# Performance work log

Hardware: AMD Instinct MI355X
Metric: run time of the kernel (lower is better)

The kernel has to match this reference:

```python
import jax, jax.numpy as jnp
import numpy as np

C_IN, C_OUT = 128, 128
B, H, W = 16, 192, 192


def _conv(x, w, pad):
    # x: NCHW, w: OIHW, pad: ((ph,ph),(pw,pw))
    return jax.lax.conv_general_dilated(
        x, w, window_strides=(1, 1), padding=pad,
        dimension_numbers=('NCHW', 'OIHW', 'NCHW'))


def _diag_masks(dtype=jnp.float32):
    eye = jnp.eye(3, dtype=dtype)            # mask_19: mask[c, c] = 1
    anti = eye[::-1, :]                      # mask_37: mask[2-c, c] = 1
    return eye[None, None], anti[None, None] # broadcast to (O,I,3,3)


def setup_inputs() -> dict:
    key = jax.random.key(0)
    ks = jax.random.split(key, 6)
    return {
        'x': jax.random.normal(ks[0], (B, C_IN, H, W), dtype=jnp.float32),
        'w_square': jax.random.normal(ks[1], (C_OUT, C_IN, 3, 3), dtype=jnp.float32) * 0.05,
        'w_ver': jax.random.normal(ks[2], (C_OUT, C_IN, 3, 1), dtype=jnp.float32) * 0.05,
        'w_hor': jax.random.normal(ks[3], (C_OUT, C_IN, 1, 3), dtype=jnp.float32) * 0.05,
        'w_diag19': jax.random.normal(ks[4], (C_OUT, C_IN, 3, 3), dtype=jnp.float32) * 0.05,
        'w_diag37': jax.random.normal(ks[5], (C_OUT, C_IN, 3, 3), dtype=jnp.float32) * 0.05,
    }


def reference(x, w_square, w_ver, w_hor, w_diag19, w_diag37):
    m19, m37 = _diag_masks(x.dtype)
    out = _conv(x, w_square, ((1, 1), (1, 1)))
    out = out + _conv(x, w_ver, ((1, 1), (0, 0)))
    out = out + _conv(x, w_hor, ((0, 0), (1, 1)))
    out = out + _conv(x, w_diag19 * m19, ((1, 1), (1, 1)))
    out = out + _conv(x, w_diag37 * m37, ((1, 1), (1, 1)))
    return out
```

## Files before the change

kernel.cpp:

```cpp
#include <hip/hip_runtime.h>

#define HH 192
#define WW 192
#define HWPIX (HH * WW)
#define PLANE 5184
#define CHUNKB 20736

typedef __attribute__((ext_vector_type(8))) short bf16x8;
typedef __attribute__((ext_vector_type(4))) float f32x4;
typedef __attribute__((ext_vector_type(4))) unsigned int u32x4;

__device__ __forceinline__ unsigned f2bf(float f) {
    unsigned u = __builtin_bit_cast(unsigned, f);
    return (u + 0x7FFFu + ((u >> 16) & 1u)) >> 16;
}

__global__ void fuse_weights(const float* __restrict__ wsq, const float* __restrict__ wv,
                             const float* __restrict__ whr, const float* __restrict__ w19,
                             const float* __restrict__ w37, unsigned short* __restrict__ wbuf) {
    int idx = blockIdx.x * 256 + threadIdx.x;
    if (idx >= 128 * 128 * 9) return;
    int o = idx / 1152;
    int r = idx - o * 1152;
    int c = r / 9;
    int tap = r - c * 9;
    int kh = tap / 3, kw = tap - kh * 3;
    float v = wsq[((o * 128 + c) * 3 + kh) * 3 + kw];
    if (kw == 1) v += wv[(o * 128 + c) * 3 + kh];
    if (kh == 1) v += whr[(o * 128 + c) * 3 + kw];
    if (kh == kw) v += w19[((o * 128 + c) * 3 + kh) * 3 + kw];
    if (kh + kw == 2) v += w37[((o * 128 + c) * 3 + kh) * 3 + kw];
    int cc = c >> 5;
    int mi = o >> 6, mo = (o >> 4) & 3;
    int ln = ((c >> 3) & 3) * 16 + (o & 15);
    int j = c & 7;
    int frag = ((cc * 3 + kw) * 2 + mi) * 12 + kh * 4 + mo;
    wbuf[(size_t)frag * 512 + ln * 8 + j] = (unsigned short)f2bf(v);
}

__global__ __launch_bounds__(256, 2) void conv1(const float* __restrict__ x,
                                                const unsigned short* __restrict__ wbuf,
                                                float* __restrict__ out) {
    __shared__ __align__(1024) unsigned char lds[2 * CHUNKB];
    const int t = threadIdx.x, l = t & 63, wvid = t >> 6;
    const int mi = wvid >> 1, ni = wvid & 1, l15 = l & 15, l4 = l >> 4;

    int id = (int)blockIdx.x;
    int id2 = (id & 7) * 288 + (id >> 3);
    int b = id2 / 144;
    int rem = id2 - b * 144;
    int by = rem / 12, bx = rem - by * 12;
    const int h0 = by * 16, w0 = bx * 16;

    const float* __restrict__ xb = x + (size_t)b * (128 * HWPIX);

    f32x4 acc[4][8];
    const f32x4 zero = {0.f, 0.f, 0.f, 0.f};
#pragma unroll
    for (int mo = 0; mo < 4; ++mo)
#pragma unroll
        for (int np = 0; np < 8; ++np) acc[mo][np] = zero;

    float sv[4][8];
    int sok[4];

#define LOADH(CC, H)                                                                    \
    _Pragma("unroll") for (int k = 0; k < 4; ++k) {                                     \
        const int item = (H) * 4 + k;                                                   \
        const int slot = item >> 1;                                                     \
        int px = (item & 1) * 256 + t;                                                  \
        if (px < 324) {                                                                 \
            int ih = px / 18, iw = px - ih * 18;                                        \
            int gh = h0 - 1 + ih, gw = w0 - 1 + iw;                                     \
            sok[k] = ((unsigned)gh < (unsigned)HH) & ((unsigned)gw < (unsigned)WW);     \
            int ghc = min(max(gh, 0), HH - 1), gwc = min(max(gw, 0), WW - 1);           \
            const float* p = xb + (size_t)((CC) * 32 + slot * 8) * HWPIX + ghc * WW + gwc; \
            _Pragma("unroll") for (int j = 0; j < 8; ++j) sv[k][j] = p[j * HWPIX];      \
        }                                                                               \
    }

#define WRITEH(H, BB)                                                                   \
    _Pragma("unroll") for (int k = 0; k < 4; ++k) {                                     \
        const int item = (H) * 4 + k;                                                   \
        const int slot = item >> 1;                                                     \
        int px = (item & 1) * 256 + t;                                                  \
        if (px < 324) {                                                                 \
            u32x4 pk;                                                                   \
            _Pragma("unroll") for (int q = 0; q < 4; ++q) {                             \
                float lo = sok[k] ? sv[k][2 * q] : 0.f;                                 \
                float hi = sok[k] ? sv[k][2 * q + 1] : 0.f;                             \
                pk[q] = f2bf(lo) | (f2bf(hi) << 16);                                    \
            }                                                                           \
            *(u32x4*)(lds + (BB) + slot * PLANE + px * 16) = pk;                        \
        }                                                                               \
    }

#define KWPASS(KW)                                                                      \
    {                                                                                   \
        const unsigned short* wp =                                                      \
            wbuf + (size_t)(((cc * 3 + (KW)) * 2 + mi) * 12) * 512 + l * 8;             \
        bf16x8 a[12];                                                                   \
        _Pragma("unroll") for (int f = 0; f < 12; ++f)                                  \
            a[f] = *(const bf16x8*)(wp + f * 512);                                      \
        _Pragma("unroll") for (int rr = 0; rr < 10; ++rr) {                             \
            bf16x8 bf = *(const bf16x8*)(lds + rdbase + (KW) * 16 + rr * 288);          \
            _Pragma("unroll") for (int kh = 0; kh < 3; ++kh) {                          \
                const int np = rr - kh;                                                 \
                if (np >= 0 && np < 8) {                                                \
                    _Pragma("unroll") for (int mo = 0; mo < 4; ++mo)                    \
                        acc[mo][np] = __builtin_amdgcn_mfma_f32_16x16x32_bf16(          \
                            a[kh * 4 + mo], bf, acc[mo][np], 0, 0, 0);                  \
                }                                                                       \
            }                                                                           \
        }                                                                               \
    }

    LOADH(0, 0)
    WRITEH(0, 0)
    LOADH(0, 1)
    WRITEH(1, 0)
    __syncthreads();

    int bb = 0;
#pragma unroll 1
    for (int cc = 0; cc < 4; ++cc) {
        const int rdbase = bb + l4 * PLANE + (ni * 144 + l15) * 16;
        if (cc < 3) { LOADH(cc + 1, 0) }
        KWPASS(0)
        if (cc < 3) {
            WRITEH(0, bb ^ CHUNKB)
            LOADH(cc + 1, 1)
        }
        KWPASS(1)
        if (cc < 3) { WRITEH(1, bb ^ CHUNKB) }
        KWPASS(2)
        __syncthreads();
        bb ^= CHUNKB;
    }

    float* __restrict__ ob = out + (size_t)b * (128 * HWPIX) + (size_t)h0 * WW + w0 + l15;
#pragma unroll
    for (int mo = 0; mo < 4; ++mo) {
#pragma unroll
        for (int j = 0; j < 4; ++j) {
            int o = mi * 64 + mo * 16 + l4 * 4 + j;
            float* op = ob + (size_t)o * HWPIX;
#pragma unroll
            for (int np = 0; np < 8; ++np)
                op[(ni * 8 + np) * WW] = acc[mo][np][j];
        }
    }
}

extern "C" void kernel_launch(void* const* d_in, const int* in_sizes, int n_in,
                              void* d_out, int out_size, void* d_ws, size_t ws_size,
                              hipStream_t stream) {
    const float* x   = (const float*)d_in[0];
    const float* wsq = (const float*)d_in[1];
    const float* wvv = (const float*)d_in[2];
    const float* wh  = (const float*)d_in[3];
    const float* w19 = (const float*)d_in[4];
    const float* w37 = (const float*)d_in[5];

    unsigned short* wbuf = (unsigned short*)d_ws;

    fuse_weights<<<576, 256, 0, stream>>>(wsq, wvv, wh, w19, w37, wbuf);
    conv1<<<2304, 256, 0, stream>>>(x, wbuf, (float*)d_out);
}
```

Before: 269.8 us.

## Vectorize halo loads as float2 pairs, swizzle LDS layout, and use packed bf16 convert

The input halo tile is now loaded as float2 pairs per thread, and the padded row width grows from 18 to 20 pixels, so global loads are wider and fewer. The work is split into three load/write phases with two register buffers, interleaved with the three kw MFMA passes. LDS writes and reads now use an XOR swizzle on 16-byte slots to avoid bank conflicts. Conversion uses the hardware v_cvt_pk_bf16_f32 instruction, and s_setprio raises wave priority during the MFMA loops. In exchange, LDS footprint and address arithmetic grow, and register pressure from the double staging buffers may limit occupancy.

```diff
diff --git a/kernel.cpp b/kernel.cpp
--- a/kernel.cpp
+++ b/kernel.cpp
@@ -3,16 +3,24 @@
 #define HH 192
 #define WW 192
 #define HWPIX (HH * WW)
-#define PLANE 5184
-#define CHUNKB 20736
+#define ROWPX 20
+#define PLANE 5824
+#define CHUNKB (4 * PLANE)
 
 typedef __attribute__((ext_vector_type(8))) short bf16x8;
 typedef __attribute__((ext_vector_type(4))) float f32x4;
+typedef __attribute__((ext_vector_type(2))) float f32x2;
 typedef __attribute__((ext_vector_type(4))) unsigned int u32x4;
 
 __device__ __forceinline__ unsigned f2bf(float f) {
     unsigned u = __builtin_bit_cast(unsigned, f);
     return (u + 0x7FFFu + ((u >> 16) & 1u)) >> 16;
+}
+
+__device__ __forceinline__ unsigned cvtpk(float lo, float hi) {
+    unsigned r;
+    asm("v_cvt_pk_bf16_f32 %0, %1, %2" : "=v"(r) : "v"(lo), "v"(hi));
+    return r;
 }
 
 __global__ void fuse_weights(const float* __restrict__ wsq, const float* __restrict__ wv,
@@ -61,79 +69,98 @@
 #pragma unroll
         for (int np = 0; np < 8; ++np) acc[mo][np] = zero;
 
-    float sv[4][8];
-    int sok[4];
+    f32x2 svA[8], svB[8];
 
-#define LOADH(CC, H)                                                                    \
-    _Pragma("unroll") for (int k = 0; k < 4; ++k) {                                     \
-        const int item = (H) * 4 + k;                                                   \
-        const int slot = item >> 1;                                                     \
-        int px = (item & 1) * 256 + t;                                                  \
-        if (px < 324) {                                                                 \
-            int ih = px / 18, iw = px - ih * 18;                                        \
-            int gh = h0 - 1 + ih, gw = w0 - 1 + iw;                                     \
-            sok[k] = ((unsigned)gh < (unsigned)HH) & ((unsigned)gw < (unsigned)WW);     \
-            int ghc = min(max(gh, 0), HH - 1), gwc = min(max(gw, 0), WW - 1);           \
-            const float* p = xb + (size_t)((CC) * 32 + slot * 8) * HWPIX + ghc * WW + gwc; \
-            _Pragma("unroll") for (int j = 0; j < 8; ++j) sv[k][j] = p[j * HWPIX];      \
-        }                                                                               \
+#define LOADH(CC, R, SV)                                                                 \
+    if ((R) < 2 || t < 208) {                                                            \
+        int item = t + 256 * (R);                                                        \
+        int s = item / 180;                                                              \
+        int pr = item - s * 180;                                                         \
+        int row = pr / 10;                                                               \
+        int pq = pr - row * 10;                                                          \
+        int gh = h0 - 1 + row;                                                           \
+        int ghc = min(max(gh, 0), HH - 1);                                               \
+        int gwb = w0 - 2 + 2 * pq;                                                       \
+        int gwc = min(max(gwb, 0), WW - 2);                                              \
+        const float* p = xb + (size_t)((CC) * 32 + s * 8) * HWPIX + ghc * WW + gwc;      \
+        _Pragma("unroll") for (int j = 0; j < 8; ++j)                                    \
+            SV[j] = *(const f32x2*)(p + (size_t)j * HWPIX);                              \
     }
 
-#define WRITEH(H, BB)                                                                   \
-    _Pragma("unroll") for (int k = 0; k < 4; ++k) {                                     \
-        const int item = (H) * 4 + k;                                                   \
-        const int slot = item >> 1;                                                     \
-        int px = (item & 1) * 256 + t;                                                  \
-        if (px < 324) {                                                                 \
-            u32x4 pk;                                                                   \
-            _Pragma("unroll") for (int q = 0; q < 4; ++q) {                             \
-                float lo = sok[k] ? sv[k][2 * q] : 0.f;                                 \
-                float hi = sok[k] ? sv[k][2 * q + 1] : 0.f;                             \
-                pk[q] = f2bf(lo) | (f2bf(hi) << 16);                                    \
-            }                                                                           \
-            *(u32x4*)(lds + (BB) + slot * PLANE + px * 16) = pk;                        \
-        }                                                                               \
+#define WRITEH(R, BB, SV)                                                                \
+    if ((R) < 2 || t < 208) {                                                            \
+        int item = t + 256 * (R);                                                        \
+        int s = item / 180;                                                              \
+        int pr = item - s * 180;                                                         \
+        int row = pr / 10;                                                               \
+        int pq = pr - row * 10;                                                          \
+        int gh = h0 - 1 + row;                                                           \
+        bool hok = (unsigned)gh < (unsigned)HH;                                          \
+        int gwb = w0 - 2 + 2 * pq;                                                       \
+        int px0 = row * ROWPX + 2 * pq;                                                  \
+        _Pragma("unroll") for (int e = 0; e < 2; ++e) {                                  \
+            bool ok = hok && ((unsigned)(gwb + e) < (unsigned)WW);                       \
+            u32x4 pk;                                                                    \
+            _Pragma("unroll") for (int q = 0; q < 4; ++q) {                              \
+                unsigned v = cvtpk(SV[2 * q][e], SV[2 * q + 1][e]);                      \
+                pk[q] = ok ? v : 0u;                                                     \
+            }                                                                            \
+            int px = px0 + e;                                                            \
+            int hi = px >> 3;                                                            \
+            int sl = (px & 7) ^ (hi & 7);                                                \
+            *(u32x4*)(lds + (BB) + s * PLANE + hi * 128 + sl * 16) = pk;                 \
+        }                                                                                \
     }
 
-#define KWPASS(KW)                                                                      \
-    {                                                                                   \
-        const unsigned short* wp =                                                      \
-            wbuf + (size_t)(((cc * 3 + (KW)) * 2 + mi) * 12) * 512 + l * 8;             \
-        bf16x8 a[12];                                                                   \
-        _Pragma("unroll") for (int f = 0; f < 12; ++f)                                  \
-            a[f] = *(const bf16x8*)(wp + f * 512);                                      \
-        _Pragma("unroll") for (int rr = 0; rr < 10; ++rr) {                             \
-            bf16x8 bf = *(const bf16x8*)(lds + rdbase + (KW) * 16 + rr * 288);          \
-            _Pragma("unroll") for (int kh = 0; kh < 3; ++kh) {                          \
-                const int np = rr - kh;                                                 \
-                if (np >= 0 && np < 8) {                                                \
-                    _Pragma("unroll") for (int mo = 0; mo < 4; ++mo)                    \
-                        acc[mo][np] = __builtin_amdgcn_mfma_f32_16x16x32_bf16(          \
-                            a[kh * 4 + mo], bf, acc[mo][np], 0, 0, 0);                  \
-                }                                                                       \
-            }                                                                           \
-        }                                                                               \
+#define KWPASS(KW)                                                                       \
+    {                                                                                    \
+        const unsigned short* wp =                                                       \
+            wbuf + (size_t)(((cc * 3 + (KW)) * 2 + mi) * 12) * 512 + l * 8;              \
+        bf16x8 a[12];                                                                    \
+        _Pragma("unroll") for (int f = 0; f < 12; ++f)                                   \
+            a[f] = *(const bf16x8*)(wp + f * 512);                                       \
+        __builtin_amdgcn_s_setprio(1);                                                   \
+        _Pragma("unroll") for (int rr = 0; rr < 10; ++rr) {                              \
+            int px = (ni * 8 + rr) * ROWPX + (KW) + 1 + l15;                             \
+            int hi = px >> 3;                                                            \
+            int addr = bb + l4 * PLANE + hi * 128 + ((px & 7) ^ (hi & 7)) * 16;          \
+            bf16x8 bf = *(const bf16x8*)(lds + addr);                                    \
+            _Pragma("unroll") for (int kh = 0; kh < 3; ++kh) {                           \
+                const int np = rr - kh;                                                  \
+                if (np >= 0 && np < 8) {                                                 \
+                    _Pragma("unroll") for (int mo = 0; mo < 4; ++mo)                     \
+                        acc[mo][np] = __builtin_amdgcn_mfma_f32_16x16x32_bf16(           \
+                            a[kh * 4 + mo], bf, acc[mo][np], 0, 0, 0);                   \
+                }                                                                        \
+            }                                                                            \
+        }                                                                                \
+        __builtin_amdgcn_s_setprio(0);                                                   \
     }
 
-    LOADH(0, 0)
-    WRITEH(0, 0)
-    LOADH(0, 1)
-    WRITEH(1, 0)
+    LOADH(0, 0, svA)
+    WRITEH(0, 0, svA)
+    LOADH(0, 1, svA)
+    WRITEH(1, 0, svA)
+    LOADH(0, 2, svA)
+    WRITEH(2, 0, svA)
     __syncthreads();
 
     int bb = 0;
 #pragma unroll 1
     for (int cc = 0; cc < 4; ++cc) {
-        const int rdbase = bb + l4 * PLANE + (ni * 144 + l15) * 16;
-        if (cc < 3) { LOADH(cc + 1, 0) }
+        if (cc < 3) { LOADH(cc + 1, 0, svA) }
         KWPASS(0)
         if (cc < 3) {
-            WRITEH(0, bb ^ CHUNKB)
-            LOADH(cc + 1, 1)
+            LOADH(cc + 1, 1, svB)
+            WRITEH(0, bb ^ CHUNKB, svA)
         }
         KWPASS(1)
-        if (cc < 3) { WRITEH(1, bb ^ CHUNKB) }
+        if (cc < 3) {
+            LOADH(cc + 1, 2, svA)
+            WRITEH(1, bb ^ CHUNKB, svB)
+        }
         KWPASS(2)
+        if (cc < 3) { WRITEH(2, bb ^ CHUNKB, svA) }
         __syncthreads();
         bb ^= CHUNKB;
     }
```

After: 414.6 us. +53.7%, slower.

## Halve conv output tile height to raise occupancy and use packed bf16 convert

Applied to the files above, without the earlier changes.

Shrinks each block's output tile from 16x16 to 8x16 pixels, halving accumulator registers and LDS staging so three blocks can fit per CU, and doubles the grid. Input staging is reorganized into three load/write rounds with two register buffers. The float-to-bf16 conversion uses the hardware v_cvt_pk_bf16_f32 instruction instead of manual rounding. In exchange, halo overhead and per-output weight fragment loads increase.

```diff
diff --git a/kernel.cpp b/kernel.cpp
--- a/kernel.cpp
+++ b/kernel.cpp
@@ -3,8 +3,9 @@
 #define HH 192
 #define WW 192
 #define HWPIX (HH * WW)
-#define PLANE 5184
-#define CHUNKB 20736
+#define NPX 180
+#define PLANE 2880
+#define CHUNKB 11520
 
 typedef __attribute__((ext_vector_type(8))) short bf16x8;
 typedef __attribute__((ext_vector_type(4))) float f32x4;
@@ -13,6 +14,12 @@
 __device__ __forceinline__ unsigned f2bf(float f) {
     unsigned u = __builtin_bit_cast(unsigned, f);
     return (u + 0x7FFFu + ((u >> 16) & 1u)) >> 16;
+}
+
+__device__ __forceinline__ unsigned cvtpk(float lo, float hi) {
+    unsigned r;
+    asm("v_cvt_pk_bf16_f32 %0, %1, %2" : "=v"(r) : "v"(lo), "v"(hi));
+    return r;
 }
 
 __global__ void fuse_weights(const float* __restrict__ wsq, const float* __restrict__ wv,
@@ -38,7 +45,7 @@
     wbuf[(size_t)frag * 512 + ln * 8 + j] = (unsigned short)f2bf(v);
 }
 
-__global__ __launch_bounds__(256, 2) void conv1(const float* __restrict__ x,
+__global__ __launch_bounds__(256, 3) void conv1(const float* __restrict__ x,
                                                 const unsigned short* __restrict__ wbuf,
                                                 float* __restrict__ out) {
     __shared__ __align__(1024) unsigned char lds[2 * CHUNKB];
@@ -46,52 +53,54 @@
     const int mi = wvid >> 1, ni = wvid & 1, l15 = l & 15, l4 = l >> 4;
 
     int id = (int)blockIdx.x;
-    int id2 = (id & 7) * 288 + (id >> 3);
-    int b = id2 / 144;
-    int rem = id2 - b * 144;
+    int id2 = (id & 7) * 576 + (id >> 3);
+    int b = id2 / 288;
+    int rem = id2 - b * 288;
     int by = rem / 12, bx = rem - by * 12;
-    const int h0 = by * 16, w0 = bx * 16;
+    const int h0 = by * 8, w0 = bx * 16;
 
     const float* __restrict__ xb = x + (size_t)b * (128 * HWPIX);
 
-    f32x4 acc[4][8];
+    f32x4 acc[4][4];
     const f32x4 zero = {0.f, 0.f, 0.f, 0.f};
 #pragma unroll
     for (int mo = 0; mo < 4; ++mo)
 #pragma unroll
-        for (int np = 0; np < 8; ++np) acc[mo][np] = zero;
+        for (int np = 0; np < 4; ++np) acc[mo][np] = zero;
 
-    float sv[4][8];
-    int sok[4];
+    float svA[8], svB[8];
 
-#define LOADH(CC, H)                                                                    \
-    _Pragma("unroll") for (int k = 0; k < 4; ++k) {                                     \
-        const int item = (H) * 4 + k;                                                   \
-        const int slot = item >> 1;                                                     \
-        int px = (item & 1) * 256 + t;                                                  \
-        if (px < 324) {                                                                 \
-            int ih = px / 18, iw = px - ih * 18;                                        \
-            int gh = h0 - 1 + ih, gw = w0 - 1 + iw;                                     \
-            sok[k] = ((unsigned)gh < (unsigned)HH) & ((unsigned)gw < (unsigned)WW);     \
-            int ghc = min(max(gh, 0), HH - 1), gwc = min(max(gw, 0), WW - 1);           \
-            const float* p = xb + (size_t)((CC) * 32 + slot * 8) * HWPIX + ghc * WW + gwc; \
-            _Pragma("unroll") for (int j = 0; j < 8; ++j) sv[k][j] = p[j * HWPIX];      \
+#define LOADR(CC, R, SV)                                                                \
+    {                                                                                   \
+        int idx_ = t + 256 * (R);                                                       \
+        if ((R) < 2 || idx_ < 720) {                                                    \
+            int slot_ = idx_ / NPX;                                                     \
+            int px_ = idx_ - slot_ * NPX;                                               \
+            int ih_ = px_ / 18, iw_ = px_ - ih_ * 18;                                   \
+            int gh_ = h0 - 1 + ih_, gw_ = w0 - 1 + iw_;                                 \
+            int ghc_ = min(max(gh_, 0), HH - 1);                                        \
+            int gwc_ = min(max(gw_, 0), WW - 1);                                        \
+            const float* p_ =                                                           \
+                xb + (size_t)((CC) * 32 + slot_ * 8) * HWPIX + ghc_ * WW + gwc_;        \
+            _Pragma("unroll") for (int j = 0; j < 8; ++j) SV[j] = p_[(size_t)j * HWPIX]; \
         }                                                                               \
     }
 
-#define WRITEH(H, BB)                                                                   \
-    _Pragma("unroll") for (int k = 0; k < 4; ++k) {                                     \
-        const int item = (H) * 4 + k;                                                   \
-        const int slot = item >> 1;                                                     \
-        int px = (item & 1) * 256 + t;                                                  \
-        if (px < 324) {                                                                 \
+#define WRITER(R, BB, SV)                                                               \
+    {                                                                                   \
+        int idx_ = t + 256 * (R);                                                       \
+        if ((R) < 2 || idx_ < 720) {                                                    \
+            int slot_ = idx_ / NPX;                                                     \
+            int px_ = idx_ - slot_ * NPX;                                               \
+            int ih_ = px_ / 18, iw_ = px_ - ih_ * 18;                                   \
+            int gh_ = h0 - 1 + ih_, gw_ = w0 - 1 + iw_;                                 \
+            int ok_ = ((unsigned)gh_ < (unsigned)HH) & ((unsigned)gw_ < (unsigned)WW);  \
             u32x4 pk;                                                                   \
             _Pragma("unroll") for (int q = 0; q < 4; ++q) {                             \
-                float lo = sok[k] ? sv[k][2 * q] : 0.f;                                 \
-                float hi = sok[k] ? sv[k][2 * q + 1] : 0.f;                             \
-                pk[q] = f2bf(lo) | (f2bf(hi) << 16);                                    \
+                unsigned v_ = cvtpk(SV[2 * q], SV[2 * q + 1]);                          \
+                pk[q] = ok_ ? v_ : 0u;                                                  \
             }                                                                           \
-            *(u32x4*)(lds + (BB) + slot * PLANE + px * 16) = pk;                        \
+            *(u32x4*)(lds + (BB) + slot_ * PLANE + px_ * 16) = pk;                      \
         }                                                                               \
     }
 
@@ -102,11 +111,12 @@
         bf16x8 a[12];                                                                   \
         _Pragma("unroll") for (int f = 0; f < 12; ++f)                                  \
             a[f] = *(const bf16x8*)(wp + f * 512);                                      \
-        _Pragma("unroll") for (int rr = 0; rr < 10; ++rr) {                             \
-            bf16x8 bf = *(const bf16x8*)(lds + rdbase + (KW) * 16 + rr * 288);          \
+        _Pragma("unroll") for (int rr = 0; rr < 6; ++rr) {                              \
+            bf16x8 bf = *(const bf16x8*)(lds + bb + l4 * PLANE +                        \
+                                         (ni * 72 + l15) * 16 + (KW) * 16 + rr * 288); \
             _Pragma("unroll") for (int kh = 0; kh < 3; ++kh) {                          \
                 const int np = rr - kh;                                                 \
-                if (np >= 0 && np < 8) {                                                \
+                if (np >= 0 && np < 4) {                                                \
                     _Pragma("unroll") for (int mo = 0; mo < 4; ++mo)                    \
                         acc[mo][np] = __builtin_amdgcn_mfma_f32_16x16x32_bf16(          \
                             a[kh * 4 + mo], bf, acc[mo][np], 0, 0, 0);                  \
@@ -115,25 +125,30 @@
         }                                                                               \
     }
 
-    LOADH(0, 0)
-    WRITEH(0, 0)
-    LOADH(0, 1)
-    WRITEH(1, 0)
+    LOADR(0, 0, svA)
+    WRITER(0, 0, svA)
+    LOADR(0, 1, svB)
+    WRITER(1, 0, svB)
+    LOADR(0, 2, svA)
+    WRITER(2, 0, svA)
     __syncthreads();
 
     int bb = 0;
 #pragma unroll 1
     for (int cc = 0; cc < 4; ++cc) {
-        const int rdbase = bb + l4 * PLANE + (ni * 144 + l15) * 16;
-        if (cc < 3) { LOADH(cc + 1, 0) }
+        if (cc < 3) { LOADR(cc + 1, 0, svA) }
         KWPASS(0)
         if (cc < 3) {
-            WRITEH(0, bb ^ CHUNKB)
-            LOADH(cc + 1, 1)
+            WRITER(0, bb ^ CHUNKB, svA)
+            LOADR(cc + 1, 1, svB)
         }
         KWPASS(1)
-        if (cc < 3) { WRITEH(1, bb ^ CHUNKB) }
+        if (cc < 3) {
+            WRITER(1, bb ^ CHUNKB, svB)
+            LOADR(cc + 1, 2, svA)
+        }
         KWPASS(2)
+        if (cc < 3) { WRITER(2, bb ^ CHUNKB, svA) }
         __syncthreads();
         bb ^= CHUNKB;
     }
@@ -146,8 +161,8 @@
             int o = mi * 64 + mo * 16 + l4 * 4 + j;
             float* op = ob + (size_t)o * HWPIX;
 #pragma unroll
-            for (int np = 0; np < 8; ++np)
-                op[(ni * 8 + np) * WW] = acc[mo][np][j];
+            for (int np = 0; np < 4; ++np)
+                op[(ni * 4 + np) * WW] = acc[mo][np][j];
         }
     }
 }
@@ -165,5 +180,5 @@
     unsigned short* wbuf = (unsigned short*)d_ws;
 
     fuse_weights<<<576, 256, 0, stream>>>(wsq, wvv, wh, w19, w37, wbuf);
-    conv1<<<2304, 256, 0, stream>>>(x, wbuf, (float*)d_out);
+    conv1<<<4608, 256, 0, stream>>>(x, wbuf, (float*)d_out);
 }
```

Measured after the change: 298.6 us. +10.7%, slower.
